# Performance work log

Measured on AMD Instinct MI355X. Metric: run time of the kernel, lower is better.

The kernel has to match this reference:

```python
import jax, jax.numpy as jnp
import numpy as np

MAX_DIST = 10
N_OUT = 8


def setup_inputs() -> dict:
    key = jax.random.key(0)
    k1, k2 = jax.random.split(key)
    B, N = 32, 512
    adjacency = jax.random.uniform(k1, (B, N, N), dtype=jnp.float32)
    node_mask = jnp.ones((B, N), dtype=bool)
    # learned embedding table: (max_distance + 2, n_out)
    emb = jax.random.normal(k2, (MAX_DIST + 2, N_OUT), dtype=jnp.float32)
    return {"adjacency": adjacency, "node_mask": node_mask, "emb": emb}


def reference(adjacency, node_mask, emb):
    # BFS distances computed under no_grad in the original -> stop_gradient
    adjacency = jax.lax.stop_gradient(adjacency)
    B, N, _ = adjacency.shape
    adj_bin = adjacency > 0.5
    adj_sym = adj_bin | jnp.swapaxes(adj_bin, -1, -2)
    pair_valid = node_mask[:, :, None] & node_mask[:, None, :]  # (B,N,N)
    adj_sym = adj_sym & pair_valid
    adj_f = adj_sym.astype(jnp.float32)

    UNREACH = MAX_DIST + 1
    eye = jnp.eye(N, dtype=bool)[None]                 # (1,N,N)
    dist = jnp.where(eye, 0, UNREACH).astype(jnp.int32)  # broadcasts to (B,N,N) later
    reach = jnp.broadcast_to(eye, (B, N, N))

    # iterative BFS: reach_{k+1} = (reach_k @ adj > 0) | reach_k
    for k in range(1, MAX_DIST + 1):
        reach_next = (jnp.einsum('bij,bjk->bik', reach.astype(jnp.float32), adj_f) > 0) | reach
        frontier = reach_next & ~reach
        dist = jnp.where(frontier, jnp.int32(k), dist)
        reach = reach_next

    dist = jnp.where(pair_valid, dist, UNREACH)  # invalid pairs -> UNREACHABLE
    return emb[dist]  # (B,N,N,n_out)
```

## Files before the change

### kernel.cpp

```cpp
#include <hip/hip_runtime.h>
#include <stdint.h>

typedef unsigned long long u64;
typedef float vf4 __attribute__((ext_vector_type(4)));

#define NB 32
#define N 512
#define MAXD 10
#define NW 8

__global__ __launch_bounds__(256) void k1_pack(const float* __restrict__ adj,
                                               const int* __restrict__ mask,
                                               u64* __restrict__ gsym) {
    __shared__ float ldsA[64 * 65];
    __shared__ float ldsB[64 * 65];
    __shared__ unsigned char mI[64], mJ[64];
    int p = blockIdx.x;
    int b = blockIdx.y;
    int ti = 0;
    while (p >= 8 - ti) { p -= 8 - ti; ++ti; }
    int tj = ti + p;
    int i0 = ti * 64, j0 = tj * 64;
    int t = threadIdx.x;
    if (t < 64) mI[t] = (mask[b * N + i0 + t] != 0);
    else if (t < 128) mJ[t - 64] = (mask[b * N + j0 + (t - 64)] != 0);
    const float* Ab = adj + (size_t)b * N * N;
    #pragma unroll
    for (int s = 0; s < 4; ++s) {
        int idx = t + 256 * s;
        int r = idx >> 4, c4 = idx & 15;
        float4 va = *(const float4*)&Ab[(size_t)(i0 + r) * N + j0 + c4 * 4];
        float4 vb = *(const float4*)&Ab[(size_t)(j0 + r) * N + i0 + c4 * 4];
        int o = r * 65 + c4 * 4;
        ldsA[o] = va.x; ldsA[o + 1] = va.y; ldsA[o + 2] = va.z; ldsA[o + 3] = va.w;
        ldsB[o] = vb.x; ldsB[o + 1] = vb.y; ldsB[o + 2] = vb.z; ldsB[o + 3] = vb.w;
    }
    __syncthreads();
    int wave = t >> 6, lane = t & 63;
    for (int s = 0; s < 16; ++s) {
        int r = wave * 16 + s;
        bool bit = ((ldsA[r * 65 + lane] > 0.5f) || (ldsB[lane * 65 + r] > 0.5f))
                   && mI[r] && mJ[lane];
        u64 word = __ballot(bit);
        if (lane == 0) gsym[((size_t)b * N + i0 + r) * NW + tj] = word;
    }
    for (int s = 0; s < 16; ++s) {
        int r = wave * 16 + s;
        bool bit = ((ldsB[r * 65 + lane] > 0.5f) || (ldsA[lane * 65 + r] > 0.5f))
                   && mJ[r] && mI[lane];
        u64 word = __ballot(bit);
        if (lane == 0) gsym[((size_t)b * N + j0 + r) * NW + ti] = word;
    }
}

__device__ __forceinline__ u64 spread8(unsigned b) {
    u64 x = (u64)(b * 0x01010101u);
    x |= x << 32;
    x &= 0x8040201008040201ULL;
    x += 0x7f7f7f7f7f7f7f7fULL;
    return (x >> 7) & 0x0101010101010101ULL;
}

__global__ __launch_bounds__(64) void k2_bfs(const u64* __restrict__ gsym,
                                             const int* __restrict__ mask,
                                             u64* __restrict__ distg64) {
    __shared__ u64 adjT[NW * N];
    __shared__ u64 outB[64 * 65];
    int blk = blockIdx.x;
    int b = blk >> 3;
    int r0 = (blk & 7) * 64;
    int t = threadIdx.x;
    const u64* gs = gsym + (size_t)b * N * NW;
    for (int q = t; q < N * NW; q += 64) {
        u64 w = gs[q];
        adjT[(q & 7) * N + (q >> 3)] = w;
    }
    __syncthreads();

    int i = r0 + t;
    bool mi = mask[b * N + i] != 0;
    u64 c0[NW], c1[NW], c2[NW], c3[NW];
    #pragma unroll
    for (int w = 0; w < NW; ++w) { c0[w] = 0; c1[w] = 0; c2[w] = 0; c3[w] = 0; }

    if (mi) {
        u64 reach[NW] = {};
        u64 frontier[NW] = {};
        reach[i >> 6] = 1ULL << (i & 63);
        #pragma unroll
        for (int w = 0; w < NW; ++w) frontier[w] = reach[w];
        bool active = true;
        for (int k = 0; k <= MAXD; ++k) {
            #pragma unroll
            for (int w = 0; w < NW; ++w) {
                u64 u = ~reach[w];
                u64 t0 = c0[w] & u; c0[w] ^= u;
                u64 t1 = c1[w] & t0; c1[w] ^= t0;
                u64 t2 = c2[w] & t1; c2[w] ^= t1;
                c3[w] ^= t2;
            }
            if (k == MAXD) break;
            if (active) {
                u64 acc[NW] = {};
                bool sat = false;
                for (int w = 0; w < NW && !sat; ++w) {
                    u64 f = frontier[w];
                    while (f) {
                        int j = (w << 6) + __builtin_ctzll(f);
                        f &= f - 1;
                        #pragma unroll
                        for (int e = 0; e < NW; ++e) acc[e] |= adjT[e * N + j];
                        u64 all = acc[0];
                        #pragma unroll
                        for (int e = 1; e < NW; ++e) all &= acc[e];
                        if (all == ~0ULL) { sat = true; break; }
                    }
                }
                bool any = false;
                #pragma unroll
                for (int w = 0; w < NW; ++w) {
                    u64 nf = acc[w] & ~reach[w];
                    frontier[w] = nf;
                    reach[w] |= nf;
                    any = any || (nf != 0);
                }
                active = any;
            }
        }
    } else {
        #pragma unroll
        for (int w = 0; w < NW; ++w) { c0[w] = ~0ULL; c1[w] = ~0ULL; c3[w] = ~0ULL; }
    }

    #pragma unroll
    for (int w = 0; w < NW; ++w) {
        #pragma unroll
        for (int h = 0; h < 8; ++h) {
            unsigned b0 = (unsigned)(c0[w] >> (8 * h)) & 0xFF;
            unsigned b1 = (unsigned)(c1[w] >> (8 * h)) & 0xFF;
            unsigned b2 = (unsigned)(c2[w] >> (8 * h)) & 0xFF;
            unsigned b3 = (unsigned)(c3[w] >> (8 * h)) & 0xFF;
            u64 bytes = spread8(b0) | (spread8(b1) << 1) | (spread8(b2) << 2) | (spread8(b3) << 3);
            outB[t * 65 + w * 8 + h] = bytes;
        }
    }
    __syncthreads();
    u64* dg = distg64 + (size_t)blk * 64 * 64;
    for (int q = t; q < 64 * 64; q += 64)
        dg[q] = outB[(q >> 6) * 65 + (q & 63)];
}

__global__ __launch_bounds__(256) void k3_expand(const unsigned char* __restrict__ distg,
                                                 const float* __restrict__ emb,
                                                 vf4* __restrict__ out4) {
    __shared__ unsigned char drow[N];
    __shared__ vf4 e4[(MAXD + 2) * 2];
    int row = blockIdx.x;
    int t = threadIdx.x;
    if (t < N / 4)
        ((uint32_t*)drow)[t] = ((const uint32_t*)distg)[(size_t)row * (N / 4) + t];
    if (t >= 128 && t < 128 + (MAXD + 2) * 2)
        e4[t - 128] = ((const vf4*)emb)[t - 128];
    __syncthreads();
    size_t base = (size_t)row * (N * 2);
    #pragma unroll
    for (int s = 0; s < 4; ++s) {
        int q = t + 256 * s;
        int j = q >> 1, h = q & 1;
        int d = drow[j];
        __builtin_nontemporal_store(e4[d * 2 + h], &out4[base + q]);
    }
}

extern "C" void kernel_launch(void* const* d_in, const int* in_sizes, int n_in,
                              void* d_out, int out_size, void* d_ws, size_t ws_size,
                              hipStream_t stream) {
    const float* adj = (const float*)d_in[0];
    const int* mask = (const int*)d_in[1];
    const float* emb = (const float*)d_in[2];
    u64* gsym = (u64*)d_ws;
    unsigned char* distg = (unsigned char*)d_ws + (size_t)NB * N * NW * 8;
    k1_pack<<<dim3(36, NB), 256, 0, stream>>>(adj, mask, gsym);
    k2_bfs<<<dim3(NB * 8), 64, 0, stream>>>(gsym, mask, (u64*)distg);
    k3_expand<<<dim3(NB * N), 256, 0, stream>>>(distg, emb, (vf4*)d_out);
}
```

Measured before the change: 363.8 us.

## Fuse BFS and embedding expansion into one kernel writing output directly

The BFS kernel and the embedding-expand kernel are merged into a single 256-thread kernel. One wave runs the BFS while the other waves load the embedding table. All four waves then expand the packed distances from LDS straight to the output. This removes the intermediate distance buffer round-trip through global memory and one kernel launch. The cost is that the large output write now comes from only 256 blocks (one per BFS tile) with little occupancy, and three waves sit idle during the BFS phase.

```diff
diff --git a/kernel.cpp b/kernel.cpp
--- a/kernel.cpp
+++ b/kernel.cpp
@@ -61,114 +61,109 @@
     return (x >> 7) & 0x0101010101010101ULL;
 }
 
-__global__ __launch_bounds__(64) void k2_bfs(const u64* __restrict__ gsym,
-                                             const int* __restrict__ mask,
-                                             u64* __restrict__ distg64) {
+__global__ __launch_bounds__(256) void k23_bfs_expand(const u64* __restrict__ gsym,
+                                                      const int* __restrict__ mask,
+                                                      const float* __restrict__ emb,
+                                                      vf4* __restrict__ out4) {
     __shared__ u64 adjT[NW * N];
     __shared__ u64 outB[64 * 65];
+    __shared__ vf4 e4[(MAXD + 2) * 2];
     int blk = blockIdx.x;
     int b = blk >> 3;
     int r0 = (blk & 7) * 64;
     int t = threadIdx.x;
     const u64* gs = gsym + (size_t)b * N * NW;
-    for (int q = t; q < N * NW; q += 64) {
+    for (int q = t; q < N * NW; q += 256) {
         u64 w = gs[q];
         adjT[(q & 7) * N + (q >> 3)] = w;
     }
+    if (t >= 64 && t < 64 + (MAXD + 2) * 2)
+        e4[t - 64] = ((const vf4*)emb)[t - 64];
     __syncthreads();
 
-    int i = r0 + t;
-    bool mi = mask[b * N + i] != 0;
-    u64 c0[NW], c1[NW], c2[NW], c3[NW];
-    #pragma unroll
-    for (int w = 0; w < NW; ++w) { c0[w] = 0; c1[w] = 0; c2[w] = 0; c3[w] = 0; }
+    if (t < 64) {
+        int i = r0 + t;
+        bool mi = mask[b * N + i] != 0;
+        u64 c0[NW], c1[NW], c2[NW], c3[NW];
+        #pragma unroll
+        for (int w = 0; w < NW; ++w) { c0[w] = 0; c1[w] = 0; c2[w] = 0; c3[w] = 0; }
 
-    if (mi) {
-        u64 reach[NW] = {};
-        u64 frontier[NW] = {};
-        reach[i >> 6] = 1ULL << (i & 63);
-        #pragma unroll
-        for (int w = 0; w < NW; ++w) frontier[w] = reach[w];
-        bool active = true;
-        for (int k = 0; k <= MAXD; ++k) {
+        if (mi) {
+            u64 reach[NW] = {};
+            u64 frontier[NW] = {};
+            reach[i >> 6] = 1ULL << (i & 63);
             #pragma unroll
-            for (int w = 0; w < NW; ++w) {
-                u64 u = ~reach[w];
-                u64 t0 = c0[w] & u; c0[w] ^= u;
-                u64 t1 = c1[w] & t0; c1[w] ^= t0;
-                u64 t2 = c2[w] & t1; c2[w] ^= t1;
-                c3[w] ^= t2;
-            }
-            if (k == MAXD) break;
-            if (active) {
-                u64 acc[NW] = {};
-                bool sat = false;
-                for (int w = 0; w < NW && !sat; ++w) {
-                    u64 f = frontier[w];
-                    while (f) {
-                        int j = (w << 6) + __builtin_ctzll(f);
-                        f &= f - 1;
-                        #pragma unroll
-                        for (int e = 0; e < NW; ++e) acc[e] |= adjT[e * N + j];
-                        u64 all = acc[0];
-                        #pragma unroll
-                        for (int e = 1; e < NW; ++e) all &= acc[e];
-                        if (all == ~0ULL) { sat = true; break; }
-                    }
-                }
-                bool any = false;
+            for (int w = 0; w < NW; ++w) frontier[w] = reach[w];
+            bool active = true;
+            for (int k = 0; k <= MAXD; ++k) {
                 #pragma unroll
                 for (int w = 0; w < NW; ++w) {
-                    u64 nf = acc[w] & ~reach[w];
-                    frontier[w] = nf;
-                    reach[w] |= nf;
-                    any = any || (nf != 0);
+                    u64 u = ~reach[w];
+                    u64 t0 = c0[w] & u; c0[w] ^= u;
+                    u64 t1 = c1[w] & t0; c1[w] ^= t0;
+                    u64 t2 = c2[w] & t1; c2[w] ^= t1;
+                    c3[w] ^= t2;
                 }
-                active = any;
+                if (k == MAXD) break;
+                if (active) {
+                    u64 acc[NW] = {};
+                    bool sat = false;
+                    for (int w = 0; w < NW && !sat; ++w) {
+                        u64 f = frontier[w];
+                        while (f) {
+                            int j = (w << 6) + __builtin_ctzll(f);
+                            f &= f - 1;
+                            #pragma unroll
+                            for (int e = 0; e < NW; ++e) acc[e] |= adjT[e * N + j];
+                            u64 all = acc[0];
+                            #pragma unroll
+                            for (int e = 1; e < NW; ++e) all &= acc[e];
+                            if (all == ~0ULL) { sat = true; break; }
+                        }
+                    }
+                    bool any = false;
+                    #pragma unroll
+                    for (int w = 0; w < NW; ++w) {
+                        u64 nf = acc[w] & ~reach[w];
+                        frontier[w] = nf;
+                        reach[w] |= nf;
+                        any = any || (nf != 0);
+                    }
+                    active = any;
+                }
             }
+        } else {
+            #pragma unroll
+            for (int w = 0; w < NW; ++w) { c0[w] = ~0ULL; c1[w] = ~0ULL; c3[w] = ~0ULL; }
         }
-    } else {
+
         #pragma unroll
-        for (int w = 0; w < NW; ++w) { c0[w] = ~0ULL; c1[w] = ~0ULL; c3[w] = ~0ULL; }
-    }
-
-    #pragma unroll
-    for (int w = 0; w < NW; ++w) {
-        #pragma unroll
-        for (int h = 0; h < 8; ++h) {
-            unsigned b0 = (unsigned)(c0[w] >> (8 * h)) & 0xFF;
-            unsigned b1 = (unsigned)(c1[w] >> (8 * h)) & 0xFF;
-            unsigned b2 = (unsigned)(c2[w] >> (8 * h)) & 0xFF;
-            unsigned b3 = (unsigned)(c3[w] >> (8 * h)) & 0xFF;
-            u64 bytes = spread8(b0) | (spread8(b1) << 1) | (spread8(b2) << 2) | (spread8(b3) << 3);
-            outB[t * 65 + w * 8 + h] = bytes;
+        for (int w = 0; w < NW; ++w) {
+            #pragma unroll
+            for (int h = 0; h < 8; ++h) {
+                unsigned b0 = (unsigned)(c0[w] >> (8 * h)) & 0xFF;
+                unsigned b1 = (unsigned)(c1[w] >> (8 * h)) & 0xFF;
+                unsigned b2 = (unsigned)(c2[w] >> (8 * h)) & 0xFF;
+                unsigned b3 = (unsigned)(c3[w] >> (8 * h)) & 0xFF;
+                outB[t * 65 + w * 8 + h] =
+                    spread8(b0) | (spread8(b1) << 1) | (spread8(b2) << 2) | (spread8(b3) << 3);
+            }
         }
     }
     __syncthreads();
-    u64* dg = distg64 + (size_t)blk * 64 * 64;
-    for (int q = t; q < 64 * 64; q += 64)
-        dg[q] = outB[(q >> 6) * 65 + (q & 63)];
-}
 
-__global__ __launch_bounds__(256) void k3_expand(const unsigned char* __restrict__ distg,
-                                                 const float* __restrict__ emb,
-                                                 vf4* __restrict__ out4) {
-    __shared__ unsigned char drow[N];
-    __shared__ vf4 e4[(MAXD + 2) * 2];
-    int row = blockIdx.x;
-    int t = threadIdx.x;
-    if (t < N / 4)
-        ((uint32_t*)drow)[t] = ((const uint32_t*)distg)[(size_t)row * (N / 4) + t];
-    if (t >= 128 && t < 128 + (MAXD + 2) * 2)
-        e4[t - 128] = ((const vf4*)emb)[t - 128];
-    __syncthreads();
-    size_t base = (size_t)row * (N * 2);
-    #pragma unroll
-    for (int s = 0; s < 4; ++s) {
-        int q = t + 256 * s;
-        int j = q >> 1, h = q & 1;
-        int d = drow[j];
-        __builtin_nontemporal_store(e4[d * 2 + h], &out4[base + q]);
+    const unsigned char* db = (const unsigned char*)outB;
+    vf4* outp = out4 + ((size_t)(b * N + r0)) * (N * 2);
+    for (int r = 0; r < 64; ++r) {
+        const unsigned char* drow = db + r * 65 * 8;
+        vf4* rowp = outp + (size_t)r * (N * 2);
+        #pragma unroll
+        for (int s = 0; s < 4; ++s) {
+            int q = t + 256 * s;
+            int j = q >> 1, h = q & 1;
+            int d = drow[j];
+            __builtin_nontemporal_store(e4[d * 2 + h], &rowp[q]);
+        }
     }
 }
 
@@ -179,8 +174,6 @@
     const int* mask = (const int*)d_in[1];
     const float* emb = (const float*)d_in[2];
     u64* gsym = (u64*)d_ws;
-    unsigned char* distg = (unsigned char*)d_ws + (size_t)NB * N * NW * 8;
     k1_pack<<<dim3(36, NB), 256, 0, stream>>>(adj, mask, gsym);
-    k2_bfs<<<dim3(NB * 8), 64, 0, stream>>>(gsym, mask, (u64*)distg);
-    k3_expand<<<dim3(NB * N), 256, 0, stream>>>(distg, emb, (vf4*)d_out);
+    k23_bfs_expand<<<dim3(NB * 8), 256, 0, stream>>>(gsym, mask, emb, (vf4*)d_out);
 }
```

New measurement: 352.8 us. 1.03x faster.
